# Kernel optimization log

Measured on AMD Instinct MI355X. Metric: run time of the kernel, lower is better.

Reference implementation:

```python
import jax, jax.numpy as jnp
import numpy as np

B, TS, D, CO, DW, DC, MAX_SEQ = 16, 512, 192, 8, 4, 2, 1000


def _ln(x, g, b, eps=1e-5):
    m = x.mean(-1, keepdims=True)
    v = ((x - m) ** 2).mean(-1, keepdims=True)
    return (x - m) * jax.lax.rsqrt(v + eps) * g + b


def _conv_block(x, k, b, bg, bb, bm, bv, lg, lb):
    # x: (B,T,Cin); k: (kw,Cin,Cout). Eval-mode BatchNorm with running stats, then SiLU, then LayerNorm.
    y = jax.lax.conv_general_dilated(x, k, (1,), 'SAME', dimension_numbers=('NWC', 'WIO', 'NWC')) + b
    y = (y - bm) * jax.lax.rsqrt(bv + 1e-5) * bg + bb
    return _ln(jax.nn.silu(y), lg, lb)


def _swish(S, E, V, W1, b1, W2, b2, W3, b3):
    # S,E: (B,Tm,Ts); V: (B,Ts,CO) -> concat to (B,Tm,Ts,CO+2), tiny 3-layer SiLU MLP
    Vb = jnp.broadcast_to(V[:, None], (V.shape[0], S.shape[1], V.shape[1], V.shape[2]))
    x = jnp.concatenate([S[..., None], E[..., None], Vb], axis=-1)
    h = jax.nn.silu(x @ W1 + b1)
    h = jax.nn.silu(h @ W2 + b2)
    return h @ W3 + b3


def setup_inputs() -> dict:
    key = jax.random.key(0)
    ks = jax.random.split(key, 16)
    def nrm(i, shape, scale):
        return jax.random.normal(ks[i], shape, dtype=jnp.float32) * scale
    # durations in [2.1,2.5] -> every row sum > MAX_SEQ, so mel_len == MAX_SEQ (static shape, exactly faithful)
    duration = jax.random.uniform(ks[0], (B, TS), minval=2.1, maxval=2.5, dtype=jnp.float32)
    tokens = nrm(1, (B, TS, D), 1.0)
    src_len = jax.random.randint(ks[2], (B,), 400, TS + 1, dtype=jnp.int32)
    src_mask = jnp.arange(TS)[None, :] >= src_len[:, None]
    inp = dict(duration=duration, tokens=tokens, src_len=src_len, src_mask=src_mask,
               tgt_len=jnp.full((B,), MAX_SEQ, dtype=jnp.int32), max_src_len=TS)
    inp.update(
        cw_kernel=nrm(3, (3, D, CO), (3 * D) ** -0.5), cw_bias=jnp.zeros((CO,), jnp.float32),
        cw_bn_gamma=jnp.ones((CO,), jnp.float32), cw_bn_beta=jnp.zeros((CO,), jnp.float32),
        cw_bn_mean=jnp.zeros((CO,), jnp.float32), cw_bn_var=jnp.ones((CO,), jnp.float32),
        cw_ln_gamma=jnp.ones((CO,), jnp.float32), cw_ln_beta=jnp.zeros((CO,), jnp.float32),
        sw_W1=nrm(4, (CO + 2, DW), (CO + 2) ** -0.5), sw_b1=jnp.zeros((DW,), jnp.float32),
        sw_W2=nrm(5, (DW, DW), DW ** -0.5), sw_b2=jnp.zeros((DW,), jnp.float32),
        sw_W3=nrm(6, (DW, DW), DW ** -0.5), sw_b3=jnp.zeros((DW,), jnp.float32),
        lw_W=nrm(7, (DW * D, D), (DW * D) ** -0.5), lw_b=jnp.zeros((D,), jnp.float32),
        cc_kernel=nrm(8, (3, D, CO), (3 * D) ** -0.5), cc_bias=jnp.zeros((CO,), jnp.float32),
        cc_bn_gamma=jnp.ones((CO,), jnp.float32), cc_bn_beta=jnp.zeros((CO,), jnp.float32),
        cc_bn_mean=jnp.zeros((CO,), jnp.float32), cc_bn_var=jnp.ones((CO,), jnp.float32),
        cc_ln_gamma=jnp.ones((CO,), jnp.float32), cc_ln_beta=jnp.zeros((CO,), jnp.float32),
        sc_W1=nrm(9, (CO + 2, DC), (CO + 2) ** -0.5), sc_b1=jnp.zeros((DC,), jnp.float32),
        sc_W2=nrm(10, (DC, DC), DC ** -0.5), sc_b2=jnp.zeros((DC,), jnp.float32),
        sc_W3=nrm(11, (DC, DC), DC ** -0.5), sc_b3=jnp.zeros((DC,), jnp.float32),
        le_W=nrm(12, (DW * DC, D), (DW * DC) ** -0.5),
        ln_gamma=jnp.ones((D,), jnp.float32), ln_beta=jnp.zeros((D,), jnp.float32),
        po_W=nrm(13, (D, 2 * D), D ** -0.5),
    )
    return inp


def reference(duration, tokens, src_len, src_mask, tgt_len, max_src_len,
              cw_kernel, cw_bias, cw_bn_gamma, cw_bn_beta, cw_bn_mean, cw_bn_var, cw_ln_gamma, cw_ln_beta,
              sw_W1, sw_b1, sw_W2, sw_b2, sw_W3, sw_b3, lw_W, lw_b,
              cc_kernel, cc_bias, cc_bn_gamma, cc_bn_beta, cc_bn_mean, cc_bn_var, cc_ln_gamma, cc_ln_beta,
              sc_W1, sc_b1, sc_W2, sc_b2, sc_W3, sc_b3, le_W, ln_gamma, ln_beta, po_W):
    TM = MAX_SEQ  # static padded mel length; inputs guarantee mel_len == MAX_SEQ for every row
    mel_len = jnp.minimum(jnp.round(duration.sum(-1)).astype(jnp.int32), MAX_SEQ)  # (B,)
    mel_mask = jnp.arange(TM)[None, :] >= mel_len[:, None]               # (B,TM)
    attn_mask = src_mask[:, None, :] | mel_mask[:, :, None]              # (B,TM,TS)
    e_k = jnp.cumsum(duration, axis=1)                                   # (B,TS)
    s_k = e_k - duration
    t = jnp.arange(1, TM + 1, dtype=duration.dtype)[None, :, None]       # (1,TM,1)
    S = jnp.where(attn_mask, 0.0, t - s_k[:, None, :])                   # (B,TM,TS)
    E = jnp.where(attn_mask, 0.0, e_k[:, None, :] - t)
    Vw = _conv_block(tokens, cw_kernel, cw_bias, cw_bn_gamma, cw_bn_beta, cw_bn_mean, cw_bn_var, cw_ln_gamma, cw_ln_beta)
    Wr = _swish(S, E, Vw, sw_W1, sw_b1, sw_W2, sw_b2, sw_W3, sw_b3)      # (B,TM,TS,DW)
    Wr = jnp.where(src_mask[:, None, :, None], -jnp.inf, Wr)
    Wsm = jax.nn.softmax(Wr, axis=2)
    Wsm = jnp.where(mel_mask[:, :, None, None], 0.0, Wsm)
    Wp = Wsm.transpose(0, 3, 1, 2)                                       # (B,DW,TM,TS)
    Vc = _conv_block(tokens, cc_kernel, cc_bias, cc_bn_gamma, cc_bn_beta, cc_bn_mean, cc_bn_var, cc_ln_gamma, cc_ln_beta)
    C = _swish(S, E, Vc, sc_W1, sc_b1, sc_W2, sc_b2, sc_W3, sc_b3)       # (B,TM,TS,DC)
    A = jnp.einsum('bqtk,bkh->btqh', Wp, tokens).reshape(duration.shape[0], TM, DW * D)
    Bc = jnp.einsum('bqtk,btkp->btqp', Wp, C).reshape(duration.shape[0], TM, DW * DC)
    up = (A @ lw_W + lw_b) + Bc @ le_W                                   # (B,TM,D)
    up = _ln(up, ln_gamma, ln_beta)
    up = jnp.where(mel_mask[..., None], 0.0, up)
    out = up @ po_W                                                      # (B,TM,2D)
    return (out, ~mel_mask, mel_len, Wp, C)
```

## Files before the change

kernel.cpp:

```cpp
#include <hip/hip_runtime.h>
#include <math.h>

constexpr int NB = 16, TSZ = 512, DDIM = 192, NCO = 8, TMM = 1000;

constexpr int WS_SK  = 0;
constexpr int WS_EK  = WS_SK  + NB*TSZ;
constexpr int WS_VW1 = WS_EK  + NB*TSZ;
constexpr int WS_VC1 = WS_VW1 + NB*TSZ*4;
constexpr int WS_BC  = WS_VC1 + NB*TSZ*2;
constexpr int WS_UP  = WS_BC  + NB*TMM*8;
constexpr int WS_MT  = WS_UP  + NB*TMM*DDIM;
constexpr int WS_ML  = WS_MT  + (NB*4*DDIM*TSZ)/2;

constexpr int OUT_OUT  = 0;
constexpr int OUT_MASK = NB*TMM*2*DDIM;
constexpr int OUT_MEL  = OUT_MASK + NB*TMM;
constexpr int OUT_WP   = OUT_MEL + NB;
constexpr int OUT_C    = OUT_WP + NB*4*TMM*TSZ;

typedef short short8  __attribute__((ext_vector_type(8)));
typedef short short4b __attribute__((ext_vector_type(4)));
typedef float floatx4 __attribute__((ext_vector_type(4)));

__device__ __forceinline__ float siluf(float x){ return x / (1.f + expf(-x)); }
__device__ __forceinline__ float silu_fast(float x){
    return x * __builtin_amdgcn_rcpf(1.f + __expf(-x));
}
__device__ __forceinline__ short f2bf(float x){
    union { float f; unsigned u; } v; v.f = x;
    unsigned r = v.u + 0x7fff + ((v.u >> 16) & 1);
    return (short)(r >> 16);
}

__global__ __launch_bounds__(TSZ) void k0_scan(const float* __restrict__ dur,
                                               float* __restrict__ ws,
                                               float* __restrict__ out){
    int b = blockIdx.x, tid = threadIdx.x;
    __shared__ float buf[TSZ];
    __shared__ int smel;
    float d = dur[b*TSZ + tid];
    buf[tid] = d;
    __syncthreads();
    for (int off = 1; off < TSZ; off <<= 1){
        float v = (tid >= off) ? buf[tid - off] : 0.f;
        __syncthreads();
        buf[tid] += v;
        __syncthreads();
    }
    float ek = buf[tid];
    ws[WS_EK + b*TSZ + tid] = ek;
    ws[WS_SK + b*TSZ + tid] = ek - d;
    if (tid == 0){
        float tot = buf[TSZ-1];
        int mel = (int)rintf(tot);
        if (mel > TMM) mel = TMM;
        smel = mel;
        ((int*)(ws + WS_ML))[b] = mel;
        out[OUT_MEL + b] = (float)mel;
    }
    __syncthreads();
    int mel = smel;
    for (int t = tid; t < TMM; t += TSZ)
        out[OUT_MASK + b*TMM + t] = (t < mel) ? 1.f : 0.f;
}

__global__ __launch_bounds__(256) void k1_conv(const float* __restrict__ tokens,
    const float* __restrict__ cwk, const float* __restrict__ cwb,
    const float* __restrict__ cwg, const float* __restrict__ cwbe,
    const float* __restrict__ cwm, const float* __restrict__ cwv,
    const float* __restrict__ cwlg, const float* __restrict__ cwlb,
    const float* __restrict__ cck, const float* __restrict__ ccb,
    const float* __restrict__ ccg, const float* __restrict__ ccbe,
    const float* __restrict__ ccm, const float* __restrict__ ccv,
    const float* __restrict__ cclg, const float* __restrict__ cclb,
    const float* __restrict__ swW1, const float* __restrict__ swb1,
    const float* __restrict__ scW1, const float* __restrict__ scb1,
    float* __restrict__ ws){
    int b = blockIdx.y, s0 = blockIdx.x * 32;
    __shared__ float xt[34*DDIM];
    for (int idx = threadIdx.x; idx < 34*DDIM; idx += 256){
        int r = idx / DDIM, i = idx % DDIM;
        int s = s0 + r - 1;
        xt[idx] = (s >= 0 && s < TSZ) ? tokens[(b*TSZ + s)*DDIM + i] : 0.f;
    }
    __syncthreads();
    int sl = threadIdx.x >> 3, c = threadIdx.x & 7;
    float yw = cwb[c], yc = ccb[c];
    for (int k = 0; k < 3; k++){
        const float* xr = &xt[(sl + k)*DDIM];
        for (int i = 0; i < DDIM; i++){
            float xv = xr[i];
            yw += xv * cwk[(k*DDIM + i)*NCO + c];
            yc += xv * cck[(k*DDIM + i)*NCO + c];
        }
    }
    yw = (yw - cwm[c]) * rsqrtf(cwv[c] + 1e-5f) * cwg[c] + cwbe[c];
    yc = (yc - ccm[c]) * rsqrtf(ccv[c] + 1e-5f) * ccg[c] + ccbe[c];
    yw = siluf(yw);
    yc = siluf(yc);
    __shared__ float vwb[32][NCO], vcb[32][NCO];
    vwb[sl][c] = yw; vcb[sl][c] = yc;
    __syncthreads();
    float mw = 0.f, mc = 0.f;
    for (int j = 0; j < NCO; j++){ mw += vwb[sl][j]; mc += vcb[sl][j]; }
    mw *= (1.f/NCO); mc *= (1.f/NCO);
    float vw_ = 0.f, vc_ = 0.f;
    for (int j = 0; j < NCO; j++){
        float a = vwb[sl][j] - mw; vw_ += a*a;
        float e = vcb[sl][j] - mc; vc_ += e*e;
    }
    vw_ *= (1.f/NCO); vc_ *= (1.f/NCO);
    float lnw = (yw - mw) * rsqrtf(vw_ + 1e-5f) * cwlg[c] + cwlb[c];
    float lnc = (yc - mc) * rsqrtf(vc_ + 1e-5f) * cclg[c] + cclb[c];
    __syncthreads();
    vwb[sl][c] = lnw; vcb[sl][c] = lnc;
    __syncthreads();
    if (threadIdx.x < 32*4){
        int sl2 = threadIdx.x >> 2, j = threadIdx.x & 3;
        float acc = swb1[j];
        for (int cc2 = 0; cc2 < NCO; cc2++) acc += vwb[sl2][cc2] * swW1[(2+cc2)*4 + j];
        ws[WS_VW1 + (b*TSZ + s0 + sl2)*4 + j] = acc;
    }
    if (threadIdx.x < 32*2){
        int sl2 = threadIdx.x >> 1, j = threadIdx.x & 1;
        float acc = scb1[j];
        for (int cc2 = 0; cc2 < NCO; cc2++) acc += vcb[sl2][cc2] * scW1[(2+cc2)*2 + j];
        ws[WS_VC1 + (b*TSZ + s0 + sl2)*2 + j] = acc;
    }
}

__global__ __launch_bounds__(256) void k2_swish(const int* __restrict__ src_len,
    const float* __restrict__ swW1, const float* __restrict__ swW2,
    const float* __restrict__ swb2, const float* __restrict__ swW3,
    const float* __restrict__ swb3,
    const float* __restrict__ scW1, const float* __restrict__ scW2,
    const float* __restrict__ scb2, const float* __restrict__ scW3,
    const float* __restrict__ scb3,
    float* __restrict__ ws, float* __restrict__ out){
    int wid = threadIdx.x >> 6, lane = threadIdx.x & 63;
    int t = blockIdx.x * 4 + wid;
    int b = blockIdx.y;
    int mel = ((const int*)(ws + WS_ML))[b];
    int slen = src_len[b];
    bool tmask = (t >= mel);
    float tv = (float)(t + 1);

    float wr[8][4];
    float cv[8][2];
    float mx[4] = {-1e30f, -1e30f, -1e30f, -1e30f};

    #pragma unroll
    for (int i = 0; i < 8; i++){
        int s = i*64 + lane;
        bool smask = (s >= slen);
        bool am = smask || tmask;
        float sk = ws[WS_SK + b*TSZ + s];
        float ek = ws[WS_EK + b*TSZ + s];
        float Sv = am ? 0.f : (tv - sk);
        float Ev = am ? 0.f : (ek - tv);
        float4 vw1 = *(const float4*)&ws[WS_VW1 + (b*TSZ + s)*4];
        float2 vc1 = *(const float2*)&ws[WS_VC1 + (b*TSZ + s)*2];
        const float* vw1p = (const float*)&vw1;
        const float* vc1p = (const float*)&vc1;

        float h1[4], h2[4];
        #pragma unroll
        for (int j = 0; j < 4; j++)
            h1[j] = silu_fast(Sv*swW1[j] + Ev*swW1[4+j] + vw1p[j]);
        #pragma unroll
        for (int j = 0; j < 4; j++){
            float a = swb2[j];
            #pragma unroll
            for (int u = 0; u < 4; u++) a += h1[u]*swW2[u*4 + j];
            h2[j] = silu_fast(a);
        }
        #pragma unroll
        for (int q = 0; q < 4; q++){
            float a = swb3[q];
            #pragma unroll
            for (int u = 0; u < 4; u++) a += h2[u]*swW3[u*4 + q];
            float v = smask ? -1e30f : a;
            wr[i][q] = v;
            mx[q] = fmaxf(mx[q], v);
        }

        float c1[2], c2[2];
        #pragma unroll
        for (int j = 0; j < 2; j++)
            c1[j] = silu_fast(Sv*scW1[j] + Ev*scW1[2+j] + vc1p[j]);
        #pragma unroll
        for (int j = 0; j < 2; j++){
            float a = scb2[j];
            #pragma unroll
            for (int u = 0; u < 2; u++) a += c1[u]*scW2[u*2 + j];
            c2[j] = silu_fast(a);
        }
        #pragma unroll
        for (int p = 0; p < 2; p++){
            float a = scb3[p];
            #pragma unroll
            for (int u = 0; u < 2; u++) a += c2[u]*scW3[u*2 + p];
            cv[i][p] = a;
        }
        *(float2*)&out[OUT_C + ((size_t)(b*TMM + t)*TSZ + s)*2] =
            make_float2(cv[i][0], cv[i][1]);
    }

    #pragma unroll
    for (int q = 0; q < 4; q++)
        #pragma unroll
        for (int o = 32; o; o >>= 1)
            mx[q] = fmaxf(mx[q], __shfl_xor(mx[q], o, 64));

    float sum[4] = {0.f, 0.f, 0.f, 0.f};
    #pragma unroll
    for (int i = 0; i < 8; i++)
        #pragma unroll
        for (int q = 0; q < 4; q++){
            float p = __expf(wr[i][q] - mx[q]);
            wr[i][q] = p;
            sum[q] += p;
        }
    #pragma unroll
    for (int q = 0; q < 4; q++)
        #pragma unroll
        for (int o = 32; o; o >>= 1)
            sum[q] += __shfl_xor(sum[q], o, 64);
    float rs[4];
    #pragma unroll
    for (int q = 0; q < 4; q++) rs[q] = __builtin_amdgcn_rcpf(sum[q]);

    float bc[8] = {0.f,0.f,0.f,0.f,0.f,0.f,0.f,0.f};
    #pragma unroll
    for (int i = 0; i < 8; i++){
        int s = i*64 + lane;
        #pragma unroll
        for (int q = 0; q < 4; q++){
            float w = tmask ? 0.f : wr[i][q]*rs[q];
            out[OUT_WP + ((size_t)(b*4 + q)*TMM + t)*TSZ + s] = w;
            bc[q*2 + 0] += w*cv[i][0];
            bc[q*2 + 1] += w*cv[i][1];
        }
    }
    #pragma unroll
    for (int j = 0; j < 8; j++)
        #pragma unroll
        for (int o = 32; o; o >>= 1)
            bc[j] += __shfl_xor(bc[j], o, 64);
    if (lane == 0){
        *(float4*)&ws[WS_BC + (b*TMM + t)*8 + 0] = make_float4(bc[0], bc[1], bc[2], bc[3]);
        *(float4*)&ws[WS_BC + (b*TMM + t)*8 + 4] = make_float4(bc[4], bc[5], bc[6], bc[7]);
    }
}

__global__ __launch_bounds__(256) void k3_mgemm(const float* __restrict__ tokens,
                                                const float* __restrict__ lwW,
                                                float* __restrict__ ws){
    int b = blockIdx.z;
    int s0 = blockIdx.x * 64;
    int y = blockIdx.y;
    int q = y / 3, d0 = (y % 3) * 64;
    __shared__ short A_sm[64*200];
    __shared__ short B_sm[64*200];
    int tid = threadIdx.x;
    for (int r = 0; r < 12; r++){
        int c = tid + r*256;
        int h = c >> 4, p = c & 15;
        float4 v = *(const float4*)&lwW[((size_t)(q*DDIM + h))*DDIM + d0 + p*4];
        A_sm[(p*4+0)*200 + h] = f2bf(v.x);
        A_sm[(p*4+1)*200 + h] = f2bf(v.y);
        A_sm[(p*4+2)*200 + h] = f2bf(v.z);
        A_sm[(p*4+3)*200 + h] = f2bf(v.w);
    }
    {
        int row = tid >> 2, part = tid & 3;
        const float* src = &tokens[((size_t)b*TSZ + s0 + row)*DDIM];
        #pragma unroll
        for (int j = 0; j < 12; j++){
            int f = part + j*4;
            float4 v = *(const float4*)&src[f*4];
            short4b wv; wv.x=f2bf(v.x); wv.y=f2bf(v.y); wv.z=f2bf(v.z); wv.w=f2bf(v.w);
            *(short4b*)&B_sm[row*200 + f*4] = wv;
        }
    }
    __syncthreads();
    int w = tid >> 6, lane = tid & 63;
    int wm = (w & 1)*32, wn = (w >> 1)*32;
    int ln = lane & 15, qd = lane >> 4;
    floatx4 acc[2][2] = {};
    for (int k0 = 0; k0 < DDIM; k0 += 32){
        short8 a0 = *(short8*)&A_sm[(wm + ln)*200 + k0 + qd*8];
        short8 a1 = *(short8*)&A_sm[(wm + 16 + ln)*200 + k0 + qd*8];
        short8 b0 = *(short8*)&B_sm[(wn + ln)*200 + k0 + qd*8];
        short8 b1 = *(short8*)&B_sm[(wn + 16 + ln)*200 + k0 + qd*8];
        acc[0][0] = __builtin_amdgcn_mfma_f32_16x16x32_bf16(a0, b0, acc[0][0], 0,0,0);
        acc[0][1] = __builtin_amdgcn_mfma_f32_16x16x32_bf16(a0, b1, acc[0][1], 0,0,0);
        acc[1][0] = __builtin_amdgcn_mfma_f32_16x16x32_bf16(a1, b0, acc[1][0], 0,0,0);
        acc[1][1] = __builtin_amdgcn_mfma_f32_16x16x32_bf16(a1, b1, acc[1][1], 0,0,0);
    }
    short* mt = (short*)(ws + WS_MT);
    #pragma unroll
    for (int mi = 0; mi < 2; mi++)
      #pragma unroll
      for (int ni = 0; ni < 2; ni++)
        #pragma unroll
        for (int r = 0; r < 4; r++){
            int d = d0 + wm + mi*16 + qd*4 + r;
            int s = s0 + wn + ni*16 + ln;
            mt[((size_t)(b*4 + q)*DDIM + d)*TSZ + s] = f2bf(acc[mi][ni][r]);
        }
}

__global__ __launch_bounds__(256) void k4_upgemm(const float* __restrict__ outbuf,
                                                 const float* __restrict__ lwb,
                                                 const float* __restrict__ leW,
                                                 float* __restrict__ ws){
    int b = blockIdx.z;
    int t0 = blockIdx.x * 64;
    int d0 = blockIdx.y * 64;
    __shared__ short A_sm[64*72];
    __shared__ short B_sm[64*72];
    const short* mt = (const short*)(ws + WS_MT);
    int tid = threadIdx.x;
    int w = tid >> 6, lane = tid & 63;
    int wm = (w & 1)*32, wn = (w >> 1)*32;
    int ln = lane & 15, qd = lane >> 4;
    floatx4 acc[2][2] = {};
    int tlA = tid >> 2, partA = tid & 3;
    for (int kc = 0; kc < 32; kc++){
        int q = kc >> 3, ss0 = (kc & 7)*64;
        {
            int t = t0 + tlA;
            if (t < TMM){
                const float* src = &outbuf[OUT_WP + ((size_t)(b*4+q)*TMM + t)*TSZ + ss0];
                #pragma unroll
                for (int j = 0; j < 4; j++){
                    int f = partA + j*4;
                    float4 v = *(const float4*)&src[f*4];
                    short4b wv; wv.x=f2bf(v.x); wv.y=f2bf(v.y); wv.z=f2bf(v.z); wv.w=f2bf(v.w);
                    *(short4b*)&A_sm[tlA*72 + f*4] = wv;
                }
            } else {
                #pragma unroll
                for (int j = 0; j < 4; j++){
                    int f = partA + j*4;
                    short4b z = {0,0,0,0};
                    *(short4b*)&A_sm[tlA*72 + f*4] = z;
                }
            }
        }
        #pragma unroll
        for (int r = 0; r < 2; r++){
            int c = tid + r*256;
            int row = c >> 3, off = c & 7;
            short8 v = *(const short8*)&mt[((size_t)(b*4+q)*DDIM + d0 + row)*TSZ + ss0 + off*8];
            *(short8*)&B_sm[row*72 + off*8] = v;
        }
        __syncthreads();
        #pragma unroll
        for (int k0 = 0; k0 < 64; k0 += 32){
            short8 a0 = *(short8*)&A_sm[(wm + ln)*72 + k0 + qd*8];
            short8 a1 = *(short8*)&A_sm[(wm + 16 + ln)*72 + k0 + qd*8];
            short8 b0 = *(short8*)&B_sm[(wn + ln)*72 + k0 + qd*8];
            short8 b1 = *(short8*)&B_sm[(wn + 16 + ln)*72 + k0 + qd*8];
            acc[0][0] = __builtin_amdgcn_mfma_f32_16x16x32_bf16(a0, b0, acc[0][0], 0,0,0);
            acc[0][1] = __builtin_amdgcn_mfma_f32_16x16x32_bf16(a0, b1, acc[0][1], 0,0,0);
            acc[1][0] = __builtin_amdgcn_mfma_f32_16x16x32_bf16(a1, b0, acc[1][0], 0,0,0);
            acc[1][1] = __builtin_amdgcn_mfma_f32_16x16x32_bf16(a1, b1, acc[1][1], 0,0,0);
        }
        __syncthreads();
    }
    float le[2][8], lwbv[2];
    #pragma unroll
    for (int ni = 0; ni < 2; ni++){
        int d = d0 + wn + ni*16 + ln;
        lwbv[ni] = lwb[d];
        #pragma unroll
        for (int j = 0; j < 8; j++) le[ni][j] = leW[j*DDIM + d];
    }
    #pragma unroll
    for (int mi = 0; mi < 2; mi++){
        #pragma unroll
        for (int r = 0; r < 4; r++){
            int t = t0 + wm + mi*16 + qd*4 + r;
            if (t < TMM){
                float4 b0 = *(const float4*)&ws[WS_BC + (b*TMM + t)*8];
                float4 b1 = *(const float4*)&ws[WS_BC + (b*TMM + t)*8 + 4];
                float bcv[8] = {b0.x,b0.y,b0.z,b0.w,b1.x,b1.y,b1.z,b1.w};
                #pragma unroll
                for (int ni = 0; ni < 2; ni++){
                    int d = d0 + wn + ni*16 + ln;
                    float a = acc[mi][ni][r] + lwbv[ni];
                    #pragma unroll
                    for (int j = 0; j < 8; j++) a += bcv[j]*le[ni][j];
                    ws[WS_UP + ((size_t)b*TMM + t)*DDIM + d] = a;
                }
            }
        }
    }
}

__global__ __launch_bounds__(384) void k5_out(const float* __restrict__ lng,
                                              const float* __restrict__ lnb,
                                              const float* __restrict__ poW,
                                              const float* __restrict__ ws,
                                              float* __restrict__ out){
    int b = blockIdx.y, t0 = blockIdx.x * 16;
    int mel = ((const int*)(ws + WS_ML))[b];
    __shared__ __align__(16) float upl[16*DDIM];
    __shared__ float mrow[16], rrow[16];
    for (int idx = threadIdx.x; idx < 16*DDIM; idx += 384){
        int r = idx / DDIM, cix = idx % DDIM;
        int t = t0 + r;
        upl[idx] = (t < TMM) ? ws[WS_UP + ((size_t)b*TMM + t)*DDIM + cix] : 0.f;
    }
    __syncthreads();
    if (threadIdx.x < 16){
        int r = threadIdx.x;
        float s = 0.f;
        for (int c = 0; c < DDIM; c++) s += upl[r*DDIM + c];
        float m = s * (1.f/DDIM);
        float v = 0.f;
        for (int c = 0; c < DDIM; c++){ float a = upl[r*DDIM + c] - m; v += a*a; }
        v *= (1.f/DDIM);
        mrow[r] = m; rrow[r] = rsqrtf(v + 1e-5f);
    }
    __syncthreads();
    for (int idx = threadIdx.x; idx < 16*DDIM; idx += 384){
        int r = idx / DDIM, cix = idx % DDIM;
        upl[idx] = (upl[idx] - mrow[r]) * rrow[r] * lng[cix] + lnb[cix];
    }
    __syncthreads();
    int j = threadIdx.x;
    float acc[16] = {};
    for (int k = 0; k < DDIM; k += 4){
        float po0 = poW[(k+0)*384 + j];
        float po1 = poW[(k+1)*384 + j];
        float po2 = poW[(k+2)*384 + j];
        float po3 = poW[(k+3)*384 + j];
        #pragma unroll
        for (int r = 0; r < 16; r++){
            float4 u = *(float4*)&upl[r*DDIM + k];
            acc[r] += u.x*po0 + u.y*po1 + u.z*po2 + u.w*po3;
        }
    }
    #pragma unroll
    for (int r = 0; r < 16; r++){
        int t = t0 + r;
        if (t < TMM)
            out[OUT_OUT + ((size_t)b*TMM + t)*384 + j] = (t < mel) ? acc[r] : 0.f;
    }
}

extern "C" void kernel_launch(void* const* d_in, const int* in_sizes, int n_in,
                              void* d_out, int out_size, void* d_ws, size_t ws_size,
                              hipStream_t stream){
    const float* duration  = (const float*)d_in[0];
    const float* tokens    = (const float*)d_in[1];
    const int*   src_len   = (const int*)d_in[2];
    const float* cw_kernel = (const float*)d_in[6];
    const float* cw_bias   = (const float*)d_in[7];
    const float* cw_bng    = (const float*)d_in[8];
    const float* cw_bnb    = (const float*)d_in[9];
    const float* cw_bnm    = (const float*)d_in[10];
    const float* cw_bnv    = (const float*)d_in[11];
    const float* cw_lng    = (const float*)d_in[12];
    const float* cw_lnb    = (const float*)d_in[13];
    const float* sw_W1     = (const float*)d_in[14];
    const float* sw_b1     = (const float*)d_in[15];
    const float* sw_W2     = (const float*)d_in[16];
    const float* sw_b2     = (const float*)d_in[17];
    const float* sw_W3     = (const float*)d_in[18];
    const float* sw_b3     = (const float*)d_in[19];
    const float* lw_W      = (const float*)d_in[20];
    const float* lw_b      = (const float*)d_in[21];
    const float* cc_kernel = (const float*)d_in[22];
    const float* cc_bias   = (const float*)d_in[23];
    const float* cc_bng    = (const float*)d_in[24];
    const float* cc_bnb    = (const float*)d_in[25];
    const float* cc_bnm    = (const float*)d_in[26];
    const float* cc_bnv    = (const float*)d_in[27];
    const float* cc_lng    = (const float*)d_in[28];
    const float* cc_lnb    = (const float*)d_in[29];
    const float* sc_W1     = (const float*)d_in[30];
    const float* sc_b1     = (const float*)d_in[31];
    const float* sc_W2     = (const float*)d_in[32];
    const float* sc_b2     = (const float*)d_in[33];
    const float* sc_W3     = (const float*)d_in[34];
    const float* sc_b3     = (const float*)d_in[35];
    const float* le_W      = (const float*)d_in[36];
    const float* ln_gamma  = (const float*)d_in[37];
    const float* ln_beta   = (const float*)d_in[38];
    const float* po_W      = (const float*)d_in[39];
    float* out = (float*)d_out;
    float* ws  = (float*)d_ws;

    k0_scan<<<NB, TSZ, 0, stream>>>(duration, ws, out);
    k1_conv<<<dim3(16, NB), 256, 0, stream>>>(tokens,
        cw_kernel, cw_bias, cw_bng, cw_bnb, cw_bnm, cw_bnv, cw_lng, cw_lnb,
        cc_kernel, cc_bias, cc_bng, cc_bnb, cc_bnm, cc_bnv, cc_lng, cc_lnb,
        sw_W1, sw_b1, sc_W1, sc_b1, ws);
    k2_swish<<<dim3(250, NB), 256, 0, stream>>>(src_len,
        sw_W1, sw_W2, sw_b2, sw_W3, sw_b3,
        sc_W1, sc_W2, sc_b2, sc_W3, sc_b3, ws, out);
    k3_mgemm<<<dim3(8, 12, NB), 256, 0, stream>>>(tokens, lw_W, ws);
    k4_upgemm<<<dim3(16, 3, NB), 256, 0, stream>>>(out, lw_b, le_W, ws);
    k5_out<<<dim3(63, NB), 384, 0, stream>>>(ln_gamma, ln_beta, po_W, ws, out);
}
```

Baseline: 530.5 us.

## Rewrite output projection with bf16 MFMA tiles and split conv reduction

```diff
diff --git a/kernel.cpp b/kernel.cpp
--- a/kernel.cpp
+++ b/kernel.cpp
@@ -64,7 +64,7 @@
         out[OUT_MASK + b*TMM + t] = (t < mel) ? 1.f : 0.f;
 }
 
-__global__ __launch_bounds__(256) void k1_conv(const float* __restrict__ tokens,
+__global__ __launch_bounds__(512) void k1_conv(const float* __restrict__ tokens,
     const float* __restrict__ cwk, const float* __restrict__ cwb,
     const float* __restrict__ cwg, const float* __restrict__ cwbe,
     const float* __restrict__ cwm, const float* __restrict__ cwv,
@@ -78,28 +78,36 @@
     float* __restrict__ ws){
     int b = blockIdx.y, s0 = blockIdx.x * 32;
     __shared__ float xt[34*DDIM];
-    for (int idx = threadIdx.x; idx < 34*DDIM; idx += 256){
+    for (int idx = threadIdx.x; idx < 34*DDIM; idx += 512){
         int r = idx / DDIM, i = idx % DDIM;
         int s = s0 + r - 1;
         xt[idx] = (s >= 0 && s < TSZ) ? tokens[(b*TSZ + s)*DDIM + i] : 0.f;
     }
     __syncthreads();
-    int sl = threadIdx.x >> 3, c = threadIdx.x & 7;
-    float yw = cwb[c], yc = ccb[c];
+    int tid = threadIdx.x;
+    int tid2 = tid >> 1, h = tid & 1;
+    int sl = tid2 >> 3, c = tid2 & 7;
+    int i0 = h * 96;
+    float yw = h ? 0.f : cwb[c];
+    float yc = h ? 0.f : ccb[c];
     for (int k = 0; k < 3; k++){
-        const float* xr = &xt[(sl + k)*DDIM];
-        for (int i = 0; i < DDIM; i++){
+        const float* xr = &xt[(sl + k)*DDIM + i0];
+        const float* kw = &cwk[((size_t)(k*DDIM + i0))*NCO + c];
+        const float* kc = &cck[((size_t)(k*DDIM + i0))*NCO + c];
+        for (int i = 0; i < 96; i++){
             float xv = xr[i];
-            yw += xv * cwk[(k*DDIM + i)*NCO + c];
-            yc += xv * cck[(k*DDIM + i)*NCO + c];
-        }
-    }
+            yw += xv * kw[i*NCO];
+            yc += xv * kc[i*NCO];
+        }
+    }
+    yw += __shfl_xor(yw, 1, 64);
+    yc += __shfl_xor(yc, 1, 64);
     yw = (yw - cwm[c]) * rsqrtf(cwv[c] + 1e-5f) * cwg[c] + cwbe[c];
     yc = (yc - ccm[c]) * rsqrtf(ccv[c] + 1e-5f) * ccg[c] + ccbe[c];
     yw = siluf(yw);
     yc = siluf(yc);
     __shared__ float vwb[32][NCO], vcb[32][NCO];
-    vwb[sl][c] = yw; vcb[sl][c] = yc;
+    if (h == 0){ vwb[sl][c] = yw; vcb[sl][c] = yc; }
     __syncthreads();
     float mw = 0.f, mc = 0.f;
     for (int j = 0; j < NCO; j++){ mw += vwb[sl][j]; mc += vcb[sl][j]; }
@@ -113,16 +121,16 @@
     float lnw = (yw - mw) * rsqrtf(vw_ + 1e-5f) * cwlg[c] + cwlb[c];
     float lnc = (yc - mc) * rsqrtf(vc_ + 1e-5f) * cclg[c] + cclb[c];
     __syncthreads();
-    vwb[sl][c] = lnw; vcb[sl][c] = lnc;
-    __syncthreads();
-    if (threadIdx.x < 32*4){
-        int sl2 = threadIdx.x >> 2, j = threadIdx.x & 3;
+    if (h == 0){ vwb[sl][c] = lnw; vcb[sl][c] = lnc; }
+    __syncthreads();
+    if (tid < 32*4){
+        int sl2 = tid >> 2, j = tid & 3;
         float acc = swb1[j];
         for (int cc2 = 0; cc2 < NCO; cc2++) acc += vwb[sl2][cc2] * swW1[(2+cc2)*4 + j];
         ws[WS_VW1 + (b*TSZ + s0 + sl2)*4 + j] = acc;
     }
-    if (threadIdx.x < 32*2){
-        int sl2 = threadIdx.x >> 1, j = threadIdx.x & 1;
+    if (tid < 32*2){
+        int sl2 = tid >> 1, j = tid & 1;
         float acc = scb1[j];
         for (int cc2 = 0; cc2 < NCO; cc2++) acc += vcb[sl2][cc2] * scW1[(2+cc2)*2 + j];
         ws[WS_VC1 + (b*TSZ + s0 + sl2)*2 + j] = acc;
@@ -400,56 +408,87 @@
     }
 }
 
-__global__ __launch_bounds__(384) void k5_out(const float* __restrict__ lng,
+__global__ __launch_bounds__(256) void k5_out(const float* __restrict__ lng,
                                               const float* __restrict__ lnb,
                                               const float* __restrict__ poW,
                                               const float* __restrict__ ws,
                                               float* __restrict__ out){
-    int b = blockIdx.y, t0 = blockIdx.x * 16;
+    int b = blockIdx.z;
+    int t0 = blockIdx.x * 64;
+    int n0 = blockIdx.y * 64;
     int mel = ((const int*)(ws + WS_ML))[b];
-    __shared__ __align__(16) float upl[16*DDIM];
-    __shared__ float mrow[16], rrow[16];
-    for (int idx = threadIdx.x; idx < 16*DDIM; idx += 384){
-        int r = idx / DDIM, cix = idx % DDIM;
-        int t = t0 + r;
-        upl[idx] = (t < TMM) ? ws[WS_UP + ((size_t)b*TMM + t)*DDIM + cix] : 0.f;
-    }
-    __syncthreads();
-    if (threadIdx.x < 16){
-        int r = threadIdx.x;
-        float s = 0.f;
-        for (int c = 0; c < DDIM; c++) s += upl[r*DDIM + c];
+    __shared__ short A_sm[64*200];
+    __shared__ short B_sm[64*200];
+    int tid = threadIdx.x;
+    {
+        int row = tid >> 2, part = tid & 3;
+        int t = t0 + row;
+        float x[48];
+        if (t < TMM){
+            const float* src = &ws[WS_UP + ((size_t)b*TMM + t)*DDIM + part*48];
+            #pragma unroll
+            for (int j = 0; j < 12; j++){
+                float4 v = *(const float4*)&src[j*4];
+                x[j*4+0] = v.x; x[j*4+1] = v.y; x[j*4+2] = v.z; x[j*4+3] = v.w;
+            }
+        } else {
+            #pragma unroll
+            for (int j = 0; j < 48; j++) x[j] = 0.f;
+        }
+        float s = 0.f, sq = 0.f;
+        #pragma unroll
+        for (int j = 0; j < 48; j++){ s += x[j]; sq += x[j]*x[j]; }
+        s  += __shfl_xor(s, 1, 64);  s  += __shfl_xor(s, 2, 64);
+        sq += __shfl_xor(sq, 1, 64); sq += __shfl_xor(sq, 2, 64);
         float m = s * (1.f/DDIM);
-        float v = 0.f;
-        for (int c = 0; c < DDIM; c++){ float a = upl[r*DDIM + c] - m; v += a*a; }
-        v *= (1.f/DDIM);
-        mrow[r] = m; rrow[r] = rsqrtf(v + 1e-5f);
-    }
-    __syncthreads();
-    for (int idx = threadIdx.x; idx < 16*DDIM; idx += 384){
-        int r = idx / DDIM, cix = idx % DDIM;
-        upl[idx] = (upl[idx] - mrow[r]) * rrow[r] * lng[cix] + lnb[cix];
-    }
-    __syncthreads();
-    int j = threadIdx.x;
-    float acc[16] = {};
-    for (int k = 0; k < DDIM; k += 4){
-        float po0 = poW[(k+0)*384 + j];
-        float po1 = poW[(k+1)*384 + j];
-        float po2 = poW[(k+2)*384 + j];
-        float po3 = poW[(k+3)*384 + j];
-        #pragma unroll
-        for (int r = 0; r < 16; r++){
-            float4 u = *(float4*)&upl[r*DDIM + k];
-            acc[r] += u.x*po0 + u.y*po1 + u.z*po2 + u.w*po3;
-        }
-    }
-    #pragma unroll
-    for (int r = 0; r < 16; r++){
-        int t = t0 + r;
-        if (t < TMM)
-            out[OUT_OUT + ((size_t)b*TMM + t)*384 + j] = (t < mel) ? acc[r] : 0.f;
-    }
+        float var = sq * (1.f/DDIM) - m*m;
+        float rstd = rsqrtf(var + 1e-5f);
+        #pragma unroll
+        for (int j = 0; j < 48; j++){
+            int k = part*48 + j;
+            float a = (x[j] - m) * rstd * lng[k] + lnb[k];
+            A_sm[row*200 + k] = f2bf(a);
+        }
+    }
+    for (int r = 0; r < 12; r++){
+        int c = tid + r*256;
+        int k = c >> 4, p = c & 15;
+        float4 v = *(const float4*)&poW[(size_t)k*(2*DDIM) + n0 + p*4];
+        B_sm[(p*4+0)*200 + k] = f2bf(v.x);
+        B_sm[(p*4+1)*200 + k] = f2bf(v.y);
+        B_sm[(p*4+2)*200 + k] = f2bf(v.z);
+        B_sm[(p*4+3)*200 + k] = f2bf(v.w);
+    }
+    __syncthreads();
+    int w = tid >> 6, lane = tid & 63;
+    int wm = (w & 1)*32, wn = (w >> 1)*32;
+    int ln = lane & 15, qd = lane >> 4;
+    floatx4 acc[2][2] = {};
+    #pragma unroll
+    for (int k0 = 0; k0 < DDIM; k0 += 32){
+        short8 a0 = *(short8*)&A_sm[(wm + ln)*200 + k0 + qd*8];
+        short8 a1 = *(short8*)&A_sm[(wm + 16 + ln)*200 + k0 + qd*8];
+        short8 b0 = *(short8*)&B_sm[(wn + ln)*200 + k0 + qd*8];
+        short8 b1 = *(short8*)&B_sm[(wn + 16 + ln)*200 + k0 + qd*8];
+        acc[0][0] = __builtin_amdgcn_mfma_f32_16x16x32_bf16(a0, b0, acc[0][0], 0,0,0);
+        acc[0][1] = __builtin_amdgcn_mfma_f32_16x16x32_bf16(a0, b1, acc[0][1], 0,0,0);
+        acc[1][0] = __builtin_amdgcn_mfma_f32_16x16x32_bf16(a1, b0, acc[1][0], 0,0,0);
+        acc[1][1] = __builtin_amdgcn_mfma_f32_16x16x32_bf16(a1, b1, acc[1][1], 0,0,0);
+    }
+    #pragma unroll
+    for (int mi = 0; mi < 2; mi++)
+      #pragma unroll
+      for (int r = 0; r < 4; r++){
+        int t = t0 + wm + mi*16 + qd*4 + r;
+        if (t < TMM){
+            bool live = (t < mel);
+            #pragma unroll
+            for (int ni = 0; ni < 2; ni++){
+                int n = n0 + wn + ni*16 + ln;
+                out[OUT_OUT + ((size_t)b*TMM + t)*(2*DDIM) + n] = live ? acc[mi][ni][r] : 0.f;
+            }
+        }
+      }
 }
 
 extern "C" void kernel_launch(void* const* d_in, const int* in_sizes, int n_in,
@@ -496,7 +535,7 @@
     float* ws  = (float*)d_ws;
 
     k0_scan<<<NB, TSZ, 0, stream>>>(duration, ws, out);
-    k1_conv<<<dim3(16, NB), 256, 0, stream>>>(tokens,
+    k1_conv<<<dim3(16, NB), 512, 0, stream>>>(tokens,
         cw_kernel, cw_bias, cw_bng, cw_bnb, cw_bnm, cw_bnv, cw_lng, cw_lnb,
         cc_kernel, cc_bias, cc_bng, cc_bnb, cc_bnm, cc_bnv, cc_lng, cc_lnb,
         sw_W1, sw_b1, sc_W1, sc_b1, ws);
@@ -505,5 +544,5 @@
         sc_W1, sc_W2, sc_b2, sc_W3, sc_b3, ws, out);
     k3_mgemm<<<dim3(8, 12, NB), 256, 0, stream>>>(tokens, lw_W, ws);
     k4_upgemm<<<dim3(16, 3, NB), 256, 0, stream>>>(out, lw_b, le_W, ws);
-    k5_out<<<dim3(63, NB), 384, 0, stream>>>(ln_gamma, ln_beta, po_W, ws, out);
-}
+    k5_out<<<dim3(16, 6, NB), 256, 0, stream>>>(ln_gamma, ln_beta, po_W, ws, out);
+}
```

Measured after the change: 472.8 us. 1.12x faster.
